# Optimization experiments

Hardware: AMD Instinct MI355X
Metric: run time of the kernel (lower is better)

Reference implementation:

```python
import jax, jax.numpy as jnp
import numpy as np
from jax import lax

T = 256          # sentence length
WD, TD = 300, 100  # word/tag embedding dims
H = WD + TD      # LSTM hidden (=input) size, per module __init__
VOCAB, NTAGS = 50000, 50
MLP_H = 400


def setup_inputs() -> dict:
    key = jax.random.key(0)
    ks = jax.random.split(key, 20)
    s = 0.05  # small init scale for numerical stability
    return {
        "words": jax.random.randint(ks[0], (T,), 0, VOCAB),
        "tags": jax.random.randint(ks[1], (T,), 0, NTAGS),
        "word_emb": jax.random.normal(ks[2], (VOCAB, WD), jnp.float32),
        "tag_emb": jax.random.normal(ks[3], (NTAGS, TD), jnp.float32),
        "Wih0": jax.random.normal(ks[4], (2, 4 * H, H), jnp.float32) * s,
        "Whh0": jax.random.normal(ks[5], (2, 4 * H, H), jnp.float32) * s,
        "bih0": jax.random.normal(ks[6], (2, 4 * H), jnp.float32) * s,
        "bhh0": jax.random.normal(ks[7], (2, 4 * H), jnp.float32) * s,
        "Wih1": jax.random.normal(ks[8], (2, 4 * H, 2 * H), jnp.float32) * s,
        "Whh1": jax.random.normal(ks[9], (2, 4 * H, H), jnp.float32) * s,
        "bih1": jax.random.normal(ks[10], (2, 4 * H), jnp.float32) * s,
        "bhh1": jax.random.normal(ks[11], (2, 4 * H), jnp.float32) * s,
        "W1": jax.random.normal(ks[12], (MLP_H, 4 * H), jnp.float32) * s,
        "b1": jax.random.normal(ks[13], (MLP_H,), jnp.float32) * s,
        "W2": jax.random.normal(ks[14], (1, MLP_H), jnp.float32) * s,
        "b2": jax.random.normal(ks[15], (1,), jnp.float32) * s,
        "h0": jax.random.normal(ks[16], (2, 2, H), jnp.float32),  # [layer, dir, H]
        "c0": jax.random.normal(ks[17], (2, 2, H), jnp.float32),
    }


def _lstm_dir(xs, Wih, Whh, bih, bhh, h0, c0, reverse):
    # xs: [T, D]; torch LSTM gate order i, f, g, o
    def step(carry, xt):
        h, c = carry
        g = xt @ Wih.T + bih + h @ Whh.T + bhh  # [4H]
        i, f, gg, o = jnp.split(g, 4)
        c = jax.nn.sigmoid(f) * c + jax.nn.sigmoid(i) * jnp.tanh(gg)
        h = jax.nn.sigmoid(o) * jnp.tanh(c)
        return (h, c), h
    _, hs = lax.scan(step, (h0, c0), xs, reverse=reverse)
    return hs  # [T, H]


def _forward(words, tags, word_emb, tag_emb, Wih0, Whh0, bih0, bhh0,
             Wih1, Whh1, bih1, bhh1, W1, b1, W2, b2, h0, c0):
    x = jnp.concatenate([word_emb[words], tag_emb[tags]], axis=1)  # [T, H]
    # layer 0, both directions
    hf0 = _lstm_dir(x, Wih0[0], Whh0[0], bih0[0], bhh0[0], h0[0, 0], c0[0, 0], False)
    hb0 = _lstm_dir(x, Wih0[1], Whh0[1], bih0[1], bhh0[1], h0[0, 1], c0[0, 1], True)
    x1 = jnp.concatenate([hf0, hb0], axis=1)  # [T, 2H]
    # layer 1
    hf1 = _lstm_dir(x1, Wih1[0], Whh1[0], bih1[0], bhh1[0], h0[1, 0], c0[1, 0], False)
    hb1 = _lstm_dir(x1, Wih1[1], Whh1[1], bih1[1], bhh1[1], h0[1, 1], c0[1, 1], True)
    hvec = jnp.concatenate([hf1, hb1], axis=1)  # [T, 2H]
    # batched pairwise MLP: score(i,j) = W2 @ tanh(W1 @ [h_i; h_j] + b1) + b2
    # Split W1 so the concat is never materialized over all T^2 pairs.
    W1a, W1b = W1[:, :2 * H], W1[:, 2 * H:]
    pi = hvec @ W1a.T  # [T, MLP_H] contribution of head word i
    pj = hvec @ W1b.T  # [T, MLP_H] contribution of dependent word j
    act = jnp.tanh(pi[:, None, :] + pj[None, :, :] + b1)  # [T, T, MLP_H]
    scores = act @ W2[0] + b2[0]  # [T, T]
    # diagonal stays 0 (permutations exclude i == j; scoreTensor was zeroed)
    return scores * (1.0 - jnp.eye(T, dtype=scores.dtype))


def reference(words, tags, word_emb, tag_emb, Wih0, Whh0, bih0, bhh0,
              Wih1, Whh1, bih1, bhh1, W1, b1, W2, b2, h0, c0):
    return _forward(words, tags, word_emb, tag_emb, Wih0, Whh0, bih0, bhh0,
                    Wih1, Whh1, bih1, bhh1, W1, b1, W2, b2, h0, c0)
```

## Files before the change

kernel.cpp:

```cpp
#include <hip/hip_runtime.h>
#include <hip/hip_bf16.h>

#define T 256
#define H 400
#define G4 1600
#define WD 300
#define TD 100
#define MLP_H 400
#define NBLK_D 25
#define HB 16
#define GR 64
#define WSTR 202
#define NPAIR 200

typedef _Float16 f16;
typedef _Float16 half2t __attribute__((ext_vector_type(2)));
typedef unsigned long long u64;
typedef unsigned int u32;

__device__ __forceinline__ float fexp(float x) {
    return __builtin_amdgcn_exp2f(x * 1.4426950408889634f);
}
__device__ __forceinline__ float sigf(float x) {
    return __builtin_amdgcn_rcpf(1.0f + fexp(-x));
}
__device__ __forceinline__ float tanhf_fast(float x) {
    return 1.0f - 2.0f * __builtin_amdgcn_rcpf(1.0f + fexp(2.0f * x));
}
__device__ __forceinline__ unsigned short f16bits(f16 x) {
    union { f16 h; unsigned short u; } v; v.h = x; return v.u;
}
__device__ __forceinline__ u32 packh2(float a, float b) {
    half2t hv; hv.x = (_Float16)a; hv.y = (_Float16)b;
    return __builtin_bit_cast(u32, hv);
}

#if __has_builtin(__builtin_amdgcn_fdot2)
__device__ __forceinline__ float dot2u(u32 a, u32 b, float c) {
    return __builtin_amdgcn_fdot2(__builtin_bit_cast(half2t, a),
                                  __builtin_bit_cast(half2t, b), c, false);
}
#else
__device__ __forceinline__ float dot2u(u32 a, u32 b, float c) {
    half2t x = __builtin_bit_cast(half2t, a), y = __builtin_bit_cast(half2t, b);
    return fmaf((float)x.y, (float)y.y, fmaf((float)x.x, (float)y.x, c));
}
#endif

__device__ __forceinline__ u64 sysload(const u64* p) {
    return __hip_atomic_load(p, __ATOMIC_RELAXED, __HIP_MEMORY_SCOPE_SYSTEM);
}
__device__ __forceinline__ void sysstore(u64* p, u64 v) {
    __hip_atomic_store(p, v, __ATOMIC_RELAXED, __HIP_MEMORY_SCOPE_SYSTEM);
}

__global__ void gather_k(const int* __restrict__ words, const int* __restrict__ tags,
                         const float* __restrict__ wemb, const float* __restrict__ temb,
                         float* __restrict__ x0) {
    int t = blockIdx.x;
    int w = words[t], g = tags[t];
    for (int c = threadIdx.x; c < H; c += 128) {
        float v = (c < WD) ? wemb[w * WD + c] : temb[g * TD + (c - WD)];
        x0[t * H + c] = v;
    }
}

__global__ __launch_bounds__(256) void gemm_tn(
    const float* __restrict__ X, int ldx,
    const float* __restrict__ Wt, int ldw, int wofs,
    const float* __restrict__ bias1, const float* __restrict__ bias2,
    float* __restrict__ out, int ldo, int Rt, int K) {
    __shared__ float Xs[64][17];
    __shared__ float Ws[64][17];
    const int tid = threadIdx.x;
    const int t0 = blockIdx.x * 64, r0 = blockIdx.y * 64;
    const int lr = tid >> 2, kq = (tid & 3) * 4;
    const int ti = tid >> 4, rj = tid & 15;
    float acc[4][4] = {};
    for (int k0 = 0; k0 < K; k0 += 16) {
        float4 xv = *(const float4*)(X + (size_t)(t0 + lr) * ldx + k0 + kq);
        Xs[lr][kq + 0] = xv.x; Xs[lr][kq + 1] = xv.y;
        Xs[lr][kq + 2] = xv.z; Xs[lr][kq + 3] = xv.w;
        int r = r0 + lr;
        float4 wv = make_float4(0.f, 0.f, 0.f, 0.f);
        if (r < Rt) wv = *(const float4*)(Wt + (size_t)r * ldw + wofs + k0 + kq);
        Ws[lr][kq + 0] = wv.x; Ws[lr][kq + 1] = wv.y;
        Ws[lr][kq + 2] = wv.z; Ws[lr][kq + 3] = wv.w;
        __syncthreads();
#pragma unroll
        for (int k = 0; k < 16; k++) {
            float xr[4], wr[4];
#pragma unroll
            for (int m = 0; m < 4; m++) xr[m] = Xs[ti * 4 + m][k];
#pragma unroll
            for (int n = 0; n < 4; n++) wr[n] = Ws[rj * 4 + n][k];
#pragma unroll
            for (int m = 0; m < 4; m++)
#pragma unroll
                for (int n = 0; n < 4; n++)
                    acc[m][n] = fmaf(xr[m], wr[n], acc[m][n]);
        }
        __syncthreads();
    }
    int rq = r0 + rj * 4;
    if (rq < Rt) {
        float b[4];
#pragma unroll
        for (int n = 0; n < 4; n++) {
            int r = rq + n;
            b[n] = (bias1 ? bias1[r] : 0.f) + (bias2 ? bias2[r] : 0.f);
        }
#pragma unroll
        for (int m = 0; m < 4; m++) {
            int t = t0 + ti * 4 + m;
            float4 o;
            o.x = acc[m][0] + b[0]; o.y = acc[m][1] + b[1];
            o.z = acc[m][2] + b[2]; o.w = acc[m][3] + b[3];
            *(float4*)(out + (size_t)t * ldo + rq) = o;
        }
    }
}

__global__ void lstm_init5(const float* __restrict__ h0, u64* sA, u64* sB) {
    int tid = threadIdx.x;
    const int TOT = 2 * 2 * NPAIR;
    for (int i = tid; i < TOT; i += 256) { sA[i] = 0xFFFFULL; sB[i] = 0xFFFFULL; }
    __syncthreads();
    for (int p = tid; p < 2 * NPAIR; p += 256) {
        int d = p / NPAIR, pr = p - d * NPAIR;
        size_t off = (size_t)(d * 2 + 0) * NPAIR + pr;
        f16 a0 = (f16)h0[d * H + 2 * pr], b0 = (f16)h0[d * H + 2 * pr + 1];
        sA[off] = 0ULL | ((u64)f16bits(a0) << 16) | ((u64)f16bits(b0) << 32);
        f16 a1 = (f16)h0[2 * H + d * H + 2 * pr], b1 = (f16)h0[2 * H + d * H + 2 * pr + 1];
        sB[off] = 0ULL | ((u64)f16bits(a1) << 16) | ((u64)f16bits(b1) << 32);
    }
}

__global__ __launch_bounds__(512, 1) void lstm_layer8(
    const float* __restrict__ G,
    const float* __restrict__ Whh,
    const float* __restrict__ c0l,
    float* __restrict__ xout,
    u64* __restrict__ slots) {
    const int role = blockIdx.x;
    const int dir = role / NBLK_D, blk = role - dir * NBLK_D;
    const int tid = threadIdx.x;
    const float* Wd = Whh + (size_t)dir * G4 * H;
    const float* Gd = G + (size_t)dir * T * G4;
    u64* sd = slots + (size_t)dir * 2 * NPAIR;

    __shared__ u32 wlds[GR * WSTR];
    __shared__ __align__(16) u32 hsh[NPAIR];
    __shared__ float gsum[GR];
    __shared__ float gsh[2][GR];

    for (int idx = tid; idx < GR * 100; idx += 512) {
        int row = idx / 100, c4 = idx - row * 100;
        int g = row >> 4, r = row & 15;
        const float4* src = (const float4*)(Wd + (size_t)(g * H + blk * HB + r) * H);
        float4 f = src[c4];
        *(uint2*)&wlds[row * WSTR + c4 * 2] =
            make_uint2(packh2(f.x, f.y), packh2(f.z, f.w));
    }
    if (tid >= 448) {
        int i = tid - 448, gg = i >> 4, rr = i & 15;
        int tt0 = dir ? (T - 1) : 0;
        gsh[0][i] = Gd[(size_t)tt0 * G4 + gg * H + blk * HB + rr];
    } else if (tid < 8) {
        u64 v = sysload(sd + blk * 8 + tid);
        hsh[blk * 8 + tid] = (u32)(v >> 16);
    }
    float c = (tid < 64) ? c0l[dir * H + blk * HB + (tid & 15)] : 0.f;
    __syncthreads();

#pragma clang loop unroll(disable)
    for (int s = 0; s < T; ++s) {
        if (tid >= 256 && tid < 448) {
            int f = tid - 256;
            int widx = f + (f >= blk * 8 ? 8 : 0);
            u64* src = sd + (size_t)(s & 1) * NPAIR + widx;
            u64 v = sysload(src);
            int spins = 0;
            while ((unsigned)(v & 0xFFFFULL) != (unsigned)s) {
                if (++spins > 16384) {
                    v = __hip_atomic_fetch_add(src, 0ULL, __ATOMIC_RELAXED,
                                               __HIP_MEMORY_SCOPE_AGENT);
                } else {
                    v = sysload(src);
                }
            }
            hsh[widx] = (u32)(v >> 16);
        } else if (tid >= 448) {
            int sn = (s + 1 < T) ? (s + 1) : s;
            int tt = dir ? (T - 1 - sn) : sn;
            int i = tid - 448, gg = i >> 4, rr = i & 15;
            gsh[(s + 1) & 1][i] = Gd[(size_t)tt * G4 + gg * H + blk * HB + rr];
        }
        __syncthreads();

        if (tid < 256) {
            const int row = tid >> 2, sl = tid & 3;
            const u32* wp = &wlds[row * WSTR + sl * 50];
            const u32* hp = &hsh[sl * 50];
            float a0 = 0.f, a1 = 0.f, a2 = 0.f, a3 = 0.f;
#pragma unroll
            for (int i = 0; i < 12; ++i) {
                uint2 wv0 = *(const uint2*)&wp[4 * i];
                uint2 hv0 = *(const uint2*)&hp[4 * i];
                uint2 wv1 = *(const uint2*)&wp[4 * i + 2];
                uint2 hv1 = *(const uint2*)&hp[4 * i + 2];
                a0 = dot2u(wv0.x, hv0.x, a0);
                a1 = dot2u(wv0.y, hv0.y, a1);
                a2 = dot2u(wv1.x, hv1.x, a2);
                a3 = dot2u(wv1.y, hv1.y, a3);
            }
            {
                uint2 wv = *(const uint2*)&wp[48];
                uint2 hv = *(const uint2*)&hp[48];
                a0 = dot2u(wv.x, hv.x, a0);
                a1 = dot2u(wv.y, hv.y, a1);
            }
            float a = (a0 + a1) + (a2 + a3);
            a += __shfl_xor(a, 1);
            a += __shfl_xor(a, 2);
            if (sl == 0) gsum[row] = a;
        }
        __syncthreads();

        if (tid < 64) {
            const int r = tid & 15;
            const float* gc = gsh[s & 1];
            float iv = gsum[r]      + gc[r];
            float fv = gsum[16 + r] + gc[16 + r];
            float gv = gsum[32 + r] + gc[32 + r];
            float ov = gsum[48 + r] + gc[48 + r];
            float cn = sigf(fv) * c + sigf(iv) * tanhf_fast(gv);
            c = cn;
            float hn = sigf(ov) * tanhf_fast(cn);
            u32 hb = (u32)f16bits((f16)hn);
            u32 lo = __shfl(hb, (2 * tid) & 63);
            u32 hi = __shfl(hb, (2 * tid + 1) & 63);
            if (tid < 8) {
                u32 pk = (lo & 0xFFFFu) | (hi << 16);
                hsh[blk * 8 + tid] = pk;
                sysstore(sd + (size_t)((s + 1) & 1) * NPAIR + blk * 8 + tid,
                         (u64)(unsigned)(s + 1) | ((u64)pk << 16));
            }
            const int tt = dir ? (T - 1 - s) : s;
            if (tid < 16)
                xout[(size_t)tt * (2 * H) + dir * H + blk * HB + tid] = hn;
        }
    }
}

__global__ __launch_bounds__(256) void scores_k(
    const float* __restrict__ pi, const float* __restrict__ pj,
    const float* __restrict__ w2, const float* __restrict__ b2p,
    float* __restrict__ out) {
    __shared__ float Ps[16][401];
    __shared__ float Qs[16][401];
    __shared__ float w2s[400];
    const int tid = threadIdx.x;
    const int i0 = blockIdx.y * 16, j0 = blockIdx.x * 16;
    for (int r = 0; r < 16; r++) {
        for (int k = tid; k < MLP_H; k += 256) {
            Ps[r][k] = pi[(size_t)(i0 + r) * MLP_H + k];
            Qs[r][k] = pj[(size_t)(j0 + r) * MLP_H + k];
        }
    }
    for (int k = tid; k < MLP_H; k += 256) w2s[k] = w2[k];
    __syncthreads();
    const int ti = tid >> 4, tj = tid & 15;
    float acc = 0.f;
#pragma unroll 4
    for (int k = 0; k < MLP_H; k++) {
        float x = Ps[ti][k] + Qs[tj][k];
        acc = fmaf(w2s[k], tanhf_fast(x), acc);
    }
    const int i = i0 + ti, j = j0 + tj;
    out[(size_t)i * T + j] = (i == j) ? 0.f : (acc + b2p[0]);
}

extern "C" void kernel_launch(void* const* d_in, const int* in_sizes, int n_in,
                              void* d_out, int out_size, void* d_ws, size_t ws_size,
                              hipStream_t stream) {
    const int*   words = (const int*)d_in[0];
    const int*   tags  = (const int*)d_in[1];
    const float* wemb  = (const float*)d_in[2];
    const float* temb  = (const float*)d_in[3];
    const float* Wih0  = (const float*)d_in[4];
    const float* Whh0  = (const float*)d_in[5];
    const float* bih0  = (const float*)d_in[6];
    const float* bhh0  = (const float*)d_in[7];
    const float* Wih1  = (const float*)d_in[8];
    const float* Whh1  = (const float*)d_in[9];
    const float* bih1  = (const float*)d_in[10];
    const float* bhh1  = (const float*)d_in[11];
    const float* W1    = (const float*)d_in[12];
    const float* b1    = (const float*)d_in[13];
    const float* W2    = (const float*)d_in[14];
    const float* b2    = (const float*)d_in[15];
    const float* h0    = (const float*)d_in[16];
    const float* c0    = (const float*)d_in[17];
    float* out = (float*)d_out;

    float* W = (float*)d_ws;
    float* x0   = W;
    float* x1   = W + 102400;
    float* hvec = W + 307200;
    float* Gb   = W + 512000;
    float* pi   = W + 1331200;
    float* pj   = W + 1433600;
    u64* slotsA = (u64*)W;
    u64* slotsB = (u64*)(W + 2048);

    gather_k<<<T, 128, 0, stream>>>(words, tags, wemb, temb, x0);

    for (int d = 0; d < 2; d++) {
        gemm_tn<<<dim3(4, 25), 256, 0, stream>>>(
            x0, H, Wih0 + (size_t)d * G4 * H, H, 0,
            bih0 + d * G4, bhh0 + d * G4,
            Gb + (size_t)d * T * G4, G4, G4, H);
    }
    lstm_init5<<<1, 256, 0, stream>>>(h0, slotsA, slotsB);
    lstm_layer8<<<2 * NBLK_D, 512, 0, stream>>>(Gb, Whh0, c0, x1, slotsA);

    for (int d = 0; d < 2; d++) {
        gemm_tn<<<dim3(4, 25), 256, 0, stream>>>(
            x1, 2 * H, Wih1 + (size_t)d * G4 * (2 * H), 2 * H, 0,
            bih1 + d * G4, bhh1 + d * G4,
            Gb + (size_t)d * T * G4, G4, G4, 2 * H);
    }
    lstm_layer8<<<2 * NBLK_D, 512, 0, stream>>>(Gb, Whh1, c0 + 2 * H, hvec, slotsB);

    gemm_tn<<<dim3(4, 7), 256, 0, stream>>>(
        hvec, 2 * H, W1, G4, 0, b1, nullptr, pi, MLP_H, MLP_H, 2 * H);
    gemm_tn<<<dim3(4, 7), 256, 0, stream>>>(
        hvec, 2 * H, W1, G4, 2 * H, nullptr, nullptr, pj, MLP_H, MLP_H, 2 * H);

    scores_k<<<dim3(16, 16), 256, 0, stream>>>(pi, pj, W2, b2, out);
}
```

Measured before the change: 1.436 ms.

## Co-locate LSTM blocks on one XCC and use L2-scoped handoff slots

The LSTM grid is oversized to 194 blocks and only blocks whose index maps (via round-robin dispatch) to XCC 0 or 1 stay active. Each block records its XCC id, and when all blocks of a direction share one XCC they exchange h through separate slots using sc0 L2-level loads and stores instead of system-scope atomics. A timeout falls back to the original system-scope path. The whole per-block gate-input slice for all timesteps is also preloaded into LDS, which removes per-step global loads of G. This relies on the hardware's block-to-XCC dispatch order and adds a large LDS footprint.

```diff
diff --git a/kernel.cpp b/kernel.cpp
--- a/kernel.cpp
+++ b/kernel.cpp
@@ -12,6 +12,7 @@
 #define GR 64
 #define WSTR 202
 #define NPAIR 200
+#define LSTM_GRID 194
 
 typedef _Float16 f16;
 typedef _Float16 half2t __attribute__((ext_vector_type(2)));
@@ -52,6 +53,24 @@
 }
 __device__ __forceinline__ void sysstore(u64* p, u64 v) {
     __hip_atomic_store(p, v, __ATOMIC_RELAXED, __HIP_MEMORY_SCOPE_SYSTEM);
+}
+__device__ __forceinline__ u32 sysload32(const u32* p) {
+    return __hip_atomic_load(p, __ATOMIC_RELAXED, __HIP_MEMORY_SCOPE_SYSTEM);
+}
+__device__ __forceinline__ void sysstore32(u32* p, u32 v) {
+    __hip_atomic_store(p, v, __ATOMIC_RELAXED, __HIP_MEMORY_SCOPE_SYSTEM);
+}
+
+__device__ __forceinline__ u64 l2load(const u64* p) {
+    u64 v;
+    asm volatile("global_load_dwordx2 %0, %1, off sc0\n\t"
+                 "s_waitcnt vmcnt(0)"
+                 : "=v"(v) : "v"(p) : "memory");
+    return v;
+}
+__device__ __forceinline__ void l2store(u64* p, u64 v) {
+    asm volatile("global_store_dwordx2 %0, %1, off sc0"
+                 :: "v"(p), "v"(v) : "memory");
 }
 
 __global__ void gather_k(const int* __restrict__ words, const int* __restrict__ tags,
@@ -121,18 +140,25 @@
     }
 }
 
-__global__ void lstm_init5(const float* __restrict__ h0, u64* sA, u64* sB) {
+__global__ void lstm_init5(const float* __restrict__ h0, u64* sA, u64* sB,
+                           u64* fA, u64* fB, u32* __restrict__ claim) {
     int tid = threadIdx.x;
     const int TOT = 2 * 2 * NPAIR;
-    for (int i = tid; i < TOT; i += 256) { sA[i] = 0xFFFFULL; sB[i] = 0xFFFFULL; }
+    for (int i = tid; i < TOT; i += 256) {
+        sA[i] = 0xFFFFULL; sB[i] = 0xFFFFULL;
+        fA[i] = 0xFFFFULL; fB[i] = 0xFFFFULL;
+    }
+    for (int i = tid; i < 128; i += 256) claim[i] = 0;
     __syncthreads();
     for (int p = tid; p < 2 * NPAIR; p += 256) {
         int d = p / NPAIR, pr = p - d * NPAIR;
         size_t off = (size_t)(d * 2 + 0) * NPAIR + pr;
         f16 a0 = (f16)h0[d * H + 2 * pr], b0 = (f16)h0[d * H + 2 * pr + 1];
-        sA[off] = 0ULL | ((u64)f16bits(a0) << 16) | ((u64)f16bits(b0) << 32);
+        u64 w0 = 0ULL | ((u64)f16bits(a0) << 16) | ((u64)f16bits(b0) << 32);
+        sA[off] = w0; fA[off] = w0;
         f16 a1 = (f16)h0[2 * H + d * H + 2 * pr], b1 = (f16)h0[2 * H + d * H + 2 * pr + 1];
-        sB[off] = 0ULL | ((u64)f16bits(a1) << 16) | ((u64)f16bits(b1) << 32);
+        u64 w1 = 0ULL | ((u64)f16bits(a1) << 16) | ((u64)f16bits(b1) << 32);
+        sB[off] = w1; fB[off] = w1;
     }
 }
 
@@ -141,18 +167,32 @@
     const float* __restrict__ Whh,
     const float* __restrict__ c0l,
     float* __restrict__ xout,
-    u64* __restrict__ slots) {
-    const int role = blockIdx.x;
-    const int dir = role / NBLK_D, blk = role - dir * NBLK_D;
+    u64* __restrict__ slots,
+    u64* __restrict__ fslots,
+    u32* __restrict__ claim) {
+    const int m8 = blockIdx.x & 7, q8 = blockIdx.x >> 3;
+    if (m8 >= 2 || q8 >= NBLK_D) return;
+    const int dir = m8, blk = q8;
+    const int role = dir * NBLK_D + blk;
     const int tid = threadIdx.x;
     const float* Wd = Whh + (size_t)dir * G4 * H;
     const float* Gd = G + (size_t)dir * T * G4;
-    u64* sd = slots + (size_t)dir * 2 * NPAIR;
+    u64* sd  = slots  + (size_t)dir * 2 * NPAIR;
+    u64* fsd = fslots + (size_t)dir * 2 * NPAIR;
 
     __shared__ u32 wlds[GR * WSTR];
     __shared__ __align__(16) u32 hsh[NPAIR];
     __shared__ float gsum[GR];
-    __shared__ float gsh[2][GR];
+    __shared__ __align__(16) float gall[T * GR];
+    __shared__ int s_fast;
+    __shared__ int s_slow;
+
+    if (tid == 0) {
+        u32 x;
+        asm volatile("s_getreg_b32 %0, hwreg(HW_REG_XCC_ID, 0, 4)" : "=s"(x));
+        sysstore32(&claim[role], x + 1);
+        s_slow = 0;
+    }
 
     for (int idx = tid; idx < GR * 100; idx += 512) {
         int row = idx / 100, c4 = idx - row * 100;
@@ -162,39 +202,60 @@
         *(uint2*)&wlds[row * WSTR + c4 * 2] =
             make_uint2(packh2(f.x, f.y), packh2(f.z, f.w));
     }
-    if (tid >= 448) {
-        int i = tid - 448, gg = i >> 4, rr = i & 15;
-        int tt0 = dir ? (T - 1) : 0;
-        gsh[0][i] = Gd[(size_t)tt0 * G4 + gg * H + blk * HB + rr];
-    } else if (tid < 8) {
+    for (int idx = tid; idx < T * GR / 4; idx += 512) {
+        int t = idx >> 4, rest = idx & 15, g = rest >> 2, q = rest & 3;
+        float4 v = *(const float4*)(Gd + (size_t)t * G4 + g * H + blk * HB + q * 4);
+        *(float4*)&gall[t * GR + g * HB + q * 4] = v;
+    }
+    if (tid < 8) {
         u64 v = sysload(sd + blk * 8 + tid);
         hsh[blk * 8 + tid] = (u32)(v >> 16);
     }
+    if (tid == 0) {
+        u32 ref = 0; int ok = 1;
+        for (int i = 0; i < NBLK_D; i++) {
+            u32 v = 0; int sp = 0;
+            do { v = sysload32(&claim[dir * NBLK_D + i]); } while (v == 0 && ++sp < (1 << 20));
+            if (v == 0) { ok = 0; break; }
+            if (i == 0) ref = v; else ok &= (v == ref);
+        }
+        s_fast = ok;
+    }
     float c = (tid < 64) ? c0l[dir * H + blk * HB + (tid & 15)] : 0.f;
     __syncthreads();
+    const int fastp = s_fast;
 
 #pragma clang loop unroll(disable)
     for (int s = 0; s < T; ++s) {
         if (tid >= 256 && tid < 448) {
             int f = tid - 256;
             int widx = f + (f >= blk * 8 ? 8 : 0);
-            u64* src = sd + (size_t)(s & 1) * NPAIR + widx;
-            u64 v = sysload(src);
-            int spins = 0;
-            while ((unsigned)(v & 0xFFFFULL) != (unsigned)s) {
-                if (++spins > 16384) {
-                    v = __hip_atomic_fetch_add(src, 0ULL, __ATOMIC_RELAXED,
-                                               __HIP_MEMORY_SCOPE_AGENT);
-                } else {
-                    v = sysload(src);
+            u64 v = 0;
+            int got = 0;
+            if (fastp && !s_slow) {
+                u64* fsrc = fsd + (size_t)(s & 1) * NPAIR + widx;
+                v = l2load(fsrc);
+                int spins = 0;
+                while ((unsigned)(v & 0xFFFFULL) != (unsigned)s && spins < 4096) {
+                    v = l2load(fsrc); ++spins;
+                }
+                if ((unsigned)(v & 0xFFFFULL) == (unsigned)s) got = 1;
+                else s_slow = 1;
+            }
+            if (!got) {
+                u64* src = sd + (size_t)(s & 1) * NPAIR + widx;
+                v = sysload(src);
+                int spins = 0;
+                while ((unsigned)(v & 0xFFFFULL) != (unsigned)s) {
+                    if (++spins > 16384) {
+                        v = __hip_atomic_fetch_add(src, 0ULL, __ATOMIC_RELAXED,
+                                                   __HIP_MEMORY_SCOPE_AGENT);
+                    } else {
+                        v = sysload(src);
+                    }
                 }
             }
             hsh[widx] = (u32)(v >> 16);
-        } else if (tid >= 448) {
-            int sn = (s + 1 < T) ? (s + 1) : s;
-            int tt = dir ? (T - 1 - sn) : sn;
-            int i = tid - 448, gg = i >> 4, rr = i & 15;
-            gsh[(s + 1) & 1][i] = Gd[(size_t)tt * G4 + gg * H + blk * HB + rr];
         }
         __syncthreads();
 
@@ -229,7 +290,8 @@
 
         if (tid < 64) {
             const int r = tid & 15;
-            const float* gc = gsh[s & 1];
+            const int tt = dir ? (T - 1 - s) : s;
+            const float* gc = &gall[tt * GR];
             float iv = gsum[r]      + gc[r];
             float fv = gsum[16 + r] + gc[16 + r];
             float gv = gsum[32 + r] + gc[32 + r];
@@ -243,10 +305,11 @@
             if (tid < 8) {
                 u32 pk = (lo & 0xFFFFu) | (hi << 16);
                 hsh[blk * 8 + tid] = pk;
-                sysstore(sd + (size_t)((s + 1) & 1) * NPAIR + blk * 8 + tid,
-                         (u64)(unsigned)(s + 1) | ((u64)pk << 16));
+                u64 w = (u64)(unsigned)(s + 1) | ((u64)pk << 16);
+                size_t so = (size_t)((s + 1) & 1) * NPAIR + blk * 8 + tid;
+                if (fastp) l2store(fsd + so, w);
+                sysstore(sd + so, w);
             }
-            const int tt = dir ? (T - 1 - s) : s;
             if (tid < 16)
                 xout[(size_t)tt * (2 * H) + dir * H + blk * HB + tid] = hn;
         }
@@ -311,8 +374,12 @@
     float* Gb   = W + 512000;
     float* pi   = W + 1331200;
     float* pj   = W + 1433600;
-    u64* slotsA = (u64*)W;
-    u64* slotsB = (u64*)(W + 2048);
+    u64* slotsA  = (u64*)W;
+    u64* slotsB  = (u64*)(W + 2048);
+    u32* claimA  = (u32*)(W + 4096);
+    u32* claimB  = claimA + 64;
+    u64* fslotsA = (u64*)(W + 8192);
+    u64* fslotsB = (u64*)(W + 12288);
 
     gather_k<<<T, 128, 0, stream>>>(words, tags, wemb, temb, x0);
 
@@ -322,8 +389,8 @@
             bih0 + d * G4, bhh0 + d * G4,
             Gb + (size_t)d * T * G4, G4, G4, H);
     }
-    lstm_init5<<<1, 256, 0, stream>>>(h0, slotsA, slotsB);
-    lstm_layer8<<<2 * NBLK_D, 512, 0, stream>>>(Gb, Whh0, c0, x1, slotsA);
+    lstm_init5<<<1, 256, 0, stream>>>(h0, slotsA, slotsB, fslotsA, fslotsB, claimA);
+    lstm_layer8<<<LSTM_GRID, 512, 0, stream>>>(Gb, Whh0, c0, x1, slotsA, fslotsA, claimA);
 
     for (int d = 0; d < 2; d++) {
         gemm_tn<<<dim3(4, 25), 256, 0, stream>>>(
@@ -331,7 +398,7 @@
             bih1 + d * G4, bhh1 + d * G4,
             Gb + (size_t)d * T * G4, G4, G4, 2 * H);
     }
-    lstm_layer8<<<2 * NBLK_D, 512, 0, stream>>>(Gb, Whh1, c0 + 2 * H, hvec, slotsB);
+    lstm_layer8<<<LSTM_GRID, 512, 0, stream>>>(Gb, Whh1, c0 + 2 * H, hvec, slotsB, fslotsB, claimB);
 
     gemm_tn<<<dim3(4, 7), 256, 0, stream>>>(
         hvec, 2 * H, W1, G4, 0, b1, nullptr, pi, MLP_H, MLP_H, 2 * H);
```

Measured after the change: 2.240 ms. 56.0% more time.

## Fuse LSTM gate reduction and cell update per wave to drop a block barrier

Applied to the files above, without the earlier changes.

The four waves that compute the recurrent matvec are remapped so that each wave holds all four gates (i, f, g, o) for four hidden units. Gate sums are gathered with shuffles instead of going through shared memory, and each wave then runs the cell update and publishes its own h slice. This removes the gsum LDS round-trip and one __syncthreads per timestep. The h buffer in LDS is double-buffered so the next step's h can be written without a race, and the G prefetch is moved after the barrier. The work per step no longer passes through a single wave, which is meant to shorten the serial critical path of the recurrence.

```diff
diff --git a/kernel.cpp b/kernel.cpp
--- a/kernel.cpp
+++ b/kernel.cpp
@@ -150,8 +150,7 @@
     u64* sd = slots + (size_t)dir * 2 * NPAIR;
 
     __shared__ u32 wlds[GR * WSTR];
-    __shared__ __align__(16) u32 hsh[NPAIR];
-    __shared__ float gsum[GR];
+    __shared__ __align__(16) u32 hsh2[2][NPAIR];
     __shared__ float gsh[2][GR];
 
     for (int idx = tid; idx < GR * 100; idx += 512) {
@@ -168,9 +167,15 @@
         gsh[0][i] = Gd[(size_t)tt0 * G4 + gg * H + blk * HB + rr];
     } else if (tid < 8) {
         u64 v = sysload(sd + blk * 8 + tid);
-        hsh[blk * 8 + tid] = (u32)(v >> 16);
-    }
-    float c = (tid < 64) ? c0l[dir * H + blk * HB + (tid & 15)] : 0.f;
+        hsh2[0][blk * 8 + tid] = (u32)(v >> 16);
+    }
+    const int l  = tid & 63;
+    const int wv = tid >> 6;
+    const int sl = l & 3;
+    const int gg = l >> 4;
+    const int jj = (l >> 2) & 3;
+    float c = 0.f;
+    if (tid < 256) c = c0l[dir * H + blk * HB + wv * 4 + jj];
     __syncthreads();
 
 #pragma clang loop unroll(disable)
@@ -189,19 +194,19 @@
                     v = sysload(src);
                 }
             }
-            hsh[widx] = (u32)(v >> 16);
-        } else if (tid >= 448) {
+            hsh2[s & 1][widx] = (u32)(v >> 16);
+        }
+        __syncthreads();
+
+        if (tid >= 448) {
             int sn = (s + 1 < T) ? (s + 1) : s;
             int tt = dir ? (T - 1 - sn) : sn;
-            int i = tid - 448, gg = i >> 4, rr = i & 15;
-            gsh[(s + 1) & 1][i] = Gd[(size_t)tt * G4 + gg * H + blk * HB + rr];
-        }
-        __syncthreads();
-
-        if (tid < 256) {
-            const int row = tid >> 2, sl = tid & 3;
-            const u32* wp = &wlds[row * WSTR + sl * 50];
-            const u32* hp = &hsh[sl * 50];
+            int i = tid - 448;
+            gsh[(s + 1) & 1][i] = Gd[(size_t)tt * G4 + (i >> 4) * H + blk * HB + (i & 15)];
+        } else if (tid < 256) {
+            const int R = gg * 16 + wv * 4 + jj;
+            const u32* wp = &wlds[R * WSTR + sl * 50];
+            const u32* hp = &hsh2[s & 1][sl * 50];
             float a0 = 0.f, a1 = 0.f, a2 = 0.f, a3 = 0.f;
 #pragma unroll
             for (int i = 0; i < 12; ++i) {
@@ -215,40 +220,41 @@
                 a3 = dot2u(wv1.y, hv1.y, a3);
             }
             {
-                uint2 wv = *(const uint2*)&wp[48];
-                uint2 hv = *(const uint2*)&hp[48];
-                a0 = dot2u(wv.x, hv.x, a0);
-                a1 = dot2u(wv.y, hv.y, a1);
+                uint2 wvx = *(const uint2*)&wp[48];
+                uint2 hvx = *(const uint2*)&hp[48];
+                a0 = dot2u(wvx.x, hvx.x, a0);
+                a1 = dot2u(wvx.y, hvx.y, a1);
             }
             float a = (a0 + a1) + (a2 + a3);
             a += __shfl_xor(a, 1);
             a += __shfl_xor(a, 2);
-            if (sl == 0) gsum[row] = a;
-        }
-        __syncthreads();
-
-        if (tid < 64) {
-            const int r = tid & 15;
+            float iv = __shfl(a, 4 * jj);
+            float fv = __shfl(a, 4 * jj + 16);
+            float gv = __shfl(a, 4 * jj + 32);
+            float ov = __shfl(a, 4 * jj + 48);
+            const int ro = wv * 4 + jj;
             const float* gc = gsh[s & 1];
-            float iv = gsum[r]      + gc[r];
-            float fv = gsum[16 + r] + gc[16 + r];
-            float gv = gsum[32 + r] + gc[32 + r];
-            float ov = gsum[48 + r] + gc[48 + r];
+            iv += gc[ro]; fv += gc[16 + ro]; gv += gc[32 + ro]; ov += gc[48 + ro];
             float cn = sigf(fv) * c + sigf(iv) * tanhf_fast(gv);
             c = cn;
             float hn = sigf(ov) * tanhf_fast(cn);
             u32 hb = (u32)f16bits((f16)hn);
-            u32 lo = __shfl(hb, (2 * tid) & 63);
-            u32 hi = __shfl(hb, (2 * tid + 1) & 63);
-            if (tid < 8) {
-                u32 pk = (lo & 0xFFFFu) | (hi << 16);
-                hsh[blk * 8 + tid] = pk;
-                sysstore(sd + (size_t)((s + 1) & 1) * NPAIR + blk * 8 + tid,
-                         (u64)(unsigned)(s + 1) | ((u64)pk << 16));
+            u32 h0b = __shfl(hb, 0), h1b = __shfl(hb, 4);
+            u32 h2b = __shfl(hb, 8), h3b = __shfl(hb, 12);
+            const int tt = dir ? (T - 1 - s) : s;
+            if (sl == 0 && gg == 0)
+                xout[(size_t)tt * (2 * H) + dir * H + blk * HB + wv * 4 + jj] = hn;
+            if (l == 0) {
+                u32 pk0 = (h0b & 0xFFFFu) | (h1b << 16);
+                hsh2[(s + 1) & 1][blk * 8 + 2 * wv] = pk0;
+                sysstore(sd + (size_t)((s + 1) & 1) * NPAIR + blk * 8 + 2 * wv,
+                         (u64)(unsigned)(s + 1) | ((u64)pk0 << 16));
+            } else if (l == 1) {
+                u32 pk1 = (h2b & 0xFFFFu) | (h3b << 16);
+                hsh2[(s + 1) & 1][blk * 8 + 2 * wv + 1] = pk1;
+                sysstore(sd + (size_t)((s + 1) & 1) * NPAIR + blk * 8 + 2 * wv + 1,
+                         (u64)(unsigned)(s + 1) | ((u64)pk1 << 16));
             }
-            const int tt = dir ? (T - 1 - s) : s;
-            if (tid < 16)
-                xout[(size_t)tt * (2 * H) + dir * H + blk * HB + tid] = hn;
         }
     }
 }
```

Result: slower. 1.959 ms (+36.4%).

## Repartition LSTM recurrence into 10 blocks per direction with 1024 threads

Applied to the files above, without the earlier changes.

The persistent recurrent LSTM kernel now uses 10 workgroups per direction instead of 25, each owning 40 hidden units (160 gate rows), and runs 1024 threads per block. Thread roles are remapped: 640 threads do the dot products, 180 poll the remote h slots, and 160 prefetch input-gate values. The aim is to cut the number of blocks in the per-step cross-block handshake and the polling contention on it. In exchange each block does 2.5x more LDS-resident matvec work per step, and the W_hh tile grows to about 129 KB of LDS.

```diff
diff --git a/kernel.cpp b/kernel.cpp
--- a/kernel.cpp
+++ b/kernel.cpp
@@ -7,11 +7,13 @@
 #define WD 300
 #define TD 100
 #define MLP_H 400
-#define NBLK_D 25
-#define HB 16
-#define GR 64
+#define NBLK_D 10
+#define HB 40
+#define GR 160
 #define WSTR 202
 #define NPAIR 200
+#define OWNW 20
+#define FORW 180
 
 typedef _Float16 f16;
 typedef _Float16 half2t __attribute__((ext_vector_type(2)));
@@ -136,7 +138,7 @@
     }
 }
 
-__global__ __launch_bounds__(512, 1) void lstm_layer8(
+__global__ __launch_bounds__(1024, 1) void lstm_layer8(
     const float* __restrict__ G,
     const float* __restrict__ Whh,
     const float* __restrict__ c0l,
@@ -154,30 +156,30 @@
     __shared__ float gsum[GR];
     __shared__ float gsh[2][GR];
 
-    for (int idx = tid; idx < GR * 100; idx += 512) {
+    for (int idx = tid; idx < GR * 100; idx += 1024) {
         int row = idx / 100, c4 = idx - row * 100;
-        int g = row >> 4, r = row & 15;
+        int g = row / HB, r = row - g * HB;
         const float4* src = (const float4*)(Wd + (size_t)(g * H + blk * HB + r) * H);
         float4 f = src[c4];
         *(uint2*)&wlds[row * WSTR + c4 * 2] =
             make_uint2(packh2(f.x, f.y), packh2(f.z, f.w));
     }
-    if (tid >= 448) {
-        int i = tid - 448, gg = i >> 4, rr = i & 15;
+    if (tid >= 864) {
+        int i = tid - 864, gg = i / HB, rr = i - gg * HB;
         int tt0 = dir ? (T - 1) : 0;
         gsh[0][i] = Gd[(size_t)tt0 * G4 + gg * H + blk * HB + rr];
-    } else if (tid < 8) {
-        u64 v = sysload(sd + blk * 8 + tid);
-        hsh[blk * 8 + tid] = (u32)(v >> 16);
-    }
-    float c = (tid < 64) ? c0l[dir * H + blk * HB + (tid & 15)] : 0.f;
+    } else if (tid < OWNW) {
+        u64 v = sysload(sd + blk * OWNW + tid);
+        hsh[blk * OWNW + tid] = (u32)(v >> 16);
+    }
+    float c = (tid < HB) ? c0l[dir * H + blk * HB + tid] : 0.f;
     __syncthreads();
 
 #pragma clang loop unroll(disable)
     for (int s = 0; s < T; ++s) {
-        if (tid >= 256 && tid < 448) {
-            int f = tid - 256;
-            int widx = f + (f >= blk * 8 ? 8 : 0);
+        if (tid >= 640 && tid < 640 + FORW) {
+            int f = tid - 640;
+            int widx = f + (f >= blk * OWNW ? OWNW : 0);
             u64* src = sd + (size_t)(s & 1) * NPAIR + widx;
             u64 v = sysload(src);
             int spins = 0;
@@ -190,15 +192,15 @@
                 }
             }
             hsh[widx] = (u32)(v >> 16);
-        } else if (tid >= 448) {
+        } else if (tid >= 864) {
             int sn = (s + 1 < T) ? (s + 1) : s;
             int tt = dir ? (T - 1 - sn) : sn;
-            int i = tid - 448, gg = i >> 4, rr = i & 15;
+            int i = tid - 864, gg = i / HB, rr = i - gg * HB;
             gsh[(s + 1) & 1][i] = Gd[(size_t)tt * G4 + gg * H + blk * HB + rr];
         }
         __syncthreads();
 
-        if (tid < 256) {
+        if (tid < 640) {
             const int row = tid >> 2, sl = tid & 3;
             const u32* wp = &wlds[row * WSTR + sl * 50];
             const u32* hp = &hsh[sl * 50];
@@ -228,27 +230,28 @@
         __syncthreads();
 
         if (tid < 64) {
-            const int r = tid & 15;
+            const int r = tid;
+            const int rr = (r < HB) ? r : 0;
             const float* gc = gsh[s & 1];
-            float iv = gsum[r]      + gc[r];
-            float fv = gsum[16 + r] + gc[16 + r];
-            float gv = gsum[32 + r] + gc[32 + r];
-            float ov = gsum[48 + r] + gc[48 + r];
+            float iv = gsum[rr]           + gc[rr];
+            float fv = gsum[HB + rr]      + gc[HB + rr];
+            float gv = gsum[2 * HB + rr]  + gc[2 * HB + rr];
+            float ov = gsum[3 * HB + rr]  + gc[3 * HB + rr];
             float cn = sigf(fv) * c + sigf(iv) * tanhf_fast(gv);
-            c = cn;
+            if (r < HB) c = cn;
             float hn = sigf(ov) * tanhf_fast(cn);
             u32 hb = (u32)f16bits((f16)hn);
             u32 lo = __shfl(hb, (2 * tid) & 63);
             u32 hi = __shfl(hb, (2 * tid + 1) & 63);
-            if (tid < 8) {
+            if (tid < OWNW) {
                 u32 pk = (lo & 0xFFFFu) | (hi << 16);
-                hsh[blk * 8 + tid] = pk;
-                sysstore(sd + (size_t)((s + 1) & 1) * NPAIR + blk * 8 + tid,
+                hsh[blk * OWNW + tid] = pk;
+                sysstore(sd + (size_t)((s + 1) & 1) * NPAIR + blk * OWNW + tid,
                          (u64)(unsigned)(s + 1) | ((u64)pk << 16));
             }
             const int tt = dir ? (T - 1 - s) : s;
-            if (tid < 16)
-                xout[(size_t)tt * (2 * H) + dir * H + blk * HB + tid] = hn;
+            if (r < HB)
+                xout[(size_t)tt * (2 * H) + dir * H + blk * HB + r] = hn;
         }
     }
 }
@@ -323,7 +326,7 @@
             Gb + (size_t)d * T * G4, G4, G4, H);
     }
     lstm_init5<<<1, 256, 0, stream>>>(h0, slotsA, slotsB);
-    lstm_layer8<<<2 * NBLK_D, 512, 0, stream>>>(Gb, Whh0, c0, x1, slotsA);
+    lstm_layer8<<<2 * NBLK_D, 1024, 0, stream>>>(Gb, Whh0, c0, x1, slotsA);
 
     for (int d = 0; d < 2; d++) {
         gemm_tn<<<dim3(4, 25), 256, 0, stream>>>(
@@ -331,7 +334,7 @@
             bih1 + d * G4, bhh1 + d * G4,
             Gb + (size_t)d * T * G4, G4, G4, 2 * H);
     }
-    lstm_layer8<<<2 * NBLK_D, 512, 0, stream>>>(Gb, Whh1, c0 + 2 * H, hvec, slotsB);
+    lstm_layer8<<<2 * NBLK_D, 1024, 0, stream>>>(Gb, Whh1, c0 + 2 * H, hvec, slotsB);
 
     gemm_tn<<<dim3(4, 7), 256, 0, stream>>>(
         hvec, 2 * H, W1, G4, 0, b1, nullptr, pi, MLP_H, MLP_H, 2 * H);
```

New measurement: 1.793 ms. +24.9%, slower.
